# Optimization experiments

Hardware: AMD Instinct MI355X
Metric: run time of the kernel (lower is better)

Reference implementation:

```python
import jax, jax.numpy as jnp
import numpy as np

N = 50000          # nodes
M_UND = 500000     # undirected edges -> E = 2*M_UND directed messages
Q = 16             # num_groups
MAX_ITER = 10
BP_MAX_DIFF = 0.01


def setup_inputs() -> dict:
    key = jax.random.key(0)
    k1, k2, k3, k4 = jax.random.split(key, 4)
    u = jax.random.randint(k1, (M_UND,), 0, N)
    v = jax.random.randint(k2, (M_UND,), 0, N)
    # each undirected edge (u,v) yields directed messages u->v and v->u
    src = jnp.concatenate([u, v]).astype(jnp.int32)
    dst = jnp.concatenate([v, u]).astype(jnp.int32)
    rev = jnp.concatenate([jnp.arange(M_UND) + M_UND, jnp.arange(M_UND)]).astype(jnp.int32)
    psi0 = jax.random.uniform(k3, (N, Q), dtype=jnp.float32)
    psi0 = psi0 / psi0.sum(1, keepdims=True)
    msg0 = jax.random.uniform(k4, (2 * M_UND, Q), dtype=jnp.float32)
    msg0 = msg0 / msg0.sum(1, keepdims=True)
    c = 2.0 * M_UND / N  # mean degree
    beta = jnp.float32(np.log(Q / np.sqrt(c - 1.0) + 1.0))  # beta_ast init
    return dict(src=src, dst=dst, rev=rev, psi0=psi0, msg0=msg0, beta=beta, n_nodes=N)


def _bp_forward(src, dst, rev, psi0, msg0, beta, n_nodes):
    q = psi0.shape[1]
    n_edges = msg0.shape[0]
    mean_w = float(n_edges) / (float(n_nodes) * float(n_nodes))  # W.mean() for 0/1 weights
    expb_m1 = jnp.exp(beta) - 1.0
    h0 = (-beta * mean_w * psi0).sum(0)  # external field, shape [q]

    def step(carry, _):
        msg, psi, h, done = carry
        # S_e = 1 + psi_{src->dst} * (e^{beta*w} - 1), w == 1
        logS = jnp.log1p(msg * expb_m1)                                    # [E, q]
        node_log = jax.ops.segment_sum(logS, dst, num_segments=n_nodes)    # prod over incoming, log-domain
        # cavity update: message i->j uses all incoming to i except j->i (rev edge)
        new_msg = jax.nn.softmax(node_log[src] - logS[rev] + h, axis=-1)   # exp(h)*prod, normalized
        diff = jnp.max(jnp.abs(jax.lax.stop_gradient(new_msg) -
                               jax.lax.stop_gradient(msg)).sum(-1))
        logS2 = jnp.log1p(new_msg * expb_m1)
        node_log2 = jax.ops.segment_sum(logS2, dst, num_segments=n_nodes)
        new_psi = jax.nn.softmax(node_log2 + h, axis=-1)                    # marginals
        new_h = (-beta * mean_w * new_psi).sum(0)
        # freeze state once converged (mirrors early-return on max_diff < bp_max_diff)
        msg = jnp.where(done, msg, new_msg)
        psi = jnp.where(done, psi, new_psi)
        h = jnp.where(done, h, new_h)
        done = done | (diff < BP_MAX_DIFF)
        return (msg, psi, h, done), diff

    (msg, psi, h, done), _ = jax.lax.scan(
        step, (msg0, psi0, h0, jnp.array(False)), None, length=MAX_ITER)

    # soft modularity: (1/2m) sum_e psi_i . psi_j - sum_g (sum_i d_i psi_ig / 2m)^2
    m2 = float(n_edges)  # total directed edge weight (= 2m for unit weights)
    deg = jax.ops.segment_sum(jnp.ones((n_edges,), psi.dtype), dst, num_segments=n_nodes)
    edge_term = jnp.einsum('eq,eq->', psi[src], psi[dst]) / m2
    deg_term = jnp.sum((jnp.einsum('n,nq->q', deg, psi) / m2) ** 2)
    modularity = edge_term - deg_term
    # group-balance regularizer, scaled by sqrt(q) as in forward()
    reg = jnp.sum((psi.sum(0) / float(n_nodes) - 1.0 / q) ** 2) * np.sqrt(q)
    # mean per-node entropy of marginals, normalized by log(q)
    entropy_loss = jnp.mean(-jnp.sum(psi * jnp.log(psi + 1e-12), axis=-1)) / np.log(q)
    return psi, reg, entropy_loss, modularity


def reference(src, dst, rev, psi0, msg0, beta, n_nodes):
    return _bp_forward(src, dst, rev, psi0, msg0, beta, n_nodes)
```

## Files before the change

### kernel.cpp

```cpp
#include <hip/hip_runtime.h>

#define Q 16
#define SCAN_B 256

__device__ __forceinline__ float wsum(float v){
  #pragma unroll
  for(int o=32;o;o>>=1) v += __shfl_xor(v,o);
  return v;
}
__device__ __forceinline__ float wmaxr(float v){
  #pragma unroll
  for(int o=32;o;o>>=1) v = fmaxf(v,__shfl_xor(v,o));
  return v;
}

__global__ void __launch_bounds__(256, 4) k_edge(
    const int* __restrict__ src, const int* __restrict__ dst,
    const float* msg_in, float* msg_out,
    const float* __restrict__ nl, const float* __restrict__ hc,
    const float* __restrict__ betap,
    float* __restrict__ diffpart, const int* __restrict__ donep, int M)
{
  if (*donep) return;
  const float eb = __expf(*betap) - 1.0f;
  const int p = blockIdx.x*blockDim.x + threadIdx.x;
  float dloc = 0.0f;
  if (p < M) {
    const int u = src[p], v = dst[p];
    const float4* a  = (const float4*)(msg_in + (size_t)p*Q);
    const float4* b  = (const float4*)(msg_in + ((size_t)p + (size_t)M)*Q);
    const float4* h4 = (const float4*)hc;
    const float4* u4 = (const float4*)(nl + (size_t)u*Q);
    const float4* v4 = (const float4*)(nl + (size_t)v*Q);
    float4 a0=a[0], a1=a[1], a2=a[2], a3=a[3];
    float4 b0=b[0], b1=b[1], b2=b[2], b3=b[3];
    float4 h0=h4[0], h1=h4[1], h2=h4[2], h3=h4[3];
    float4 un0=u4[0], un1=u4[1], un2=u4[2], un3=u4[3];
    float4 vn0=v4[0], vn1=v4[1], vn2=v4[2], vn3=v4[3];
    float muv[Q], mvu[Q], hq[Q], nlu[Q], nlv[Q];
    #define UNP(arr,r0,r1,r2,r3) \
      arr[0]=r0.x;arr[1]=r0.y;arr[2]=r0.z;arr[3]=r0.w; \
      arr[4]=r1.x;arr[5]=r1.y;arr[6]=r1.z;arr[7]=r1.w; \
      arr[8]=r2.x;arr[9]=r2.y;arr[10]=r2.z;arr[11]=r2.w; \
      arr[12]=r3.x;arr[13]=r3.y;arr[14]=r3.z;arr[15]=r3.w;
    UNP(muv,a0,a1,a2,a3) UNP(mvu,b0,b1,b2,b3) UNP(hq,h0,h1,h2,h3)
    UNP(nlu,un0,un1,un2,un3) UNP(nlv,vn0,vn1,vn2,vn3)
    #undef UNP
    float tuv[Q], tvu[Q];
    #pragma unroll
    for (int q=0;q<Q;q++){
      float lsuv = __logf(fmaf(muv[q], eb, 1.0f));
      float lsvu = __logf(fmaf(mvu[q], eb, 1.0f));
      tuv[q] = nlu[q] - lsvu + hq[q];
      tvu[q] = nlv[q] - lsuv + hq[q];
    }
    float m1 = tuv[0], m2 = tvu[0];
    #pragma unroll
    for (int q=1;q<Q;q++){ m1=fmaxf(m1,tuv[q]); m2=fmaxf(m2,tvu[q]); }
    float s1=0.0f, s2=0.0f;
    #pragma unroll
    for (int q=0;q<Q;q++){
      tuv[q]=__expf(tuv[q]-m1); s1+=tuv[q];
      tvu[q]=__expf(tvu[q]-m2); s2+=tvu[q];
    }
    const float r1 = 1.0f/s1, r2 = 1.0f/s2;
    float d1=0.0f, d2=0.0f;
    #pragma unroll
    for (int q=0;q<Q;q++){
      float nuv = tuv[q]*r1, nvu = tvu[q]*r2;
      d1 += fabsf(nuv - muv[q]);
      d2 += fabsf(nvu - mvu[q]);
      muv[q]=nuv; mvu[q]=nvu;
    }
    dloc = fmaxf(d1,d2);
    float4* o1 = (float4*)(msg_out + (size_t)p*Q);
    float4* o2 = (float4*)(msg_out + ((size_t)p + (size_t)M)*Q);
    #pragma unroll
    for (int i=0;i<4;i++){
      o1[i] = make_float4(muv[4*i],muv[4*i+1],muv[4*i+2],muv[4*i+3]);
      o2[i] = make_float4(mvu[4*i],mvu[4*i+1],mvu[4*i+2],mvu[4*i+3]);
    }
  }
  __shared__ float smx[4];
  float wm = wmaxr(dloc);
  if ((threadIdx.x & 63) == 0) smx[threadIdx.x>>6] = wm;
  __syncthreads();
  if (threadIdx.x == 0)
    diffpart[blockIdx.x] = fmaxf(fmaxf(smx[0],smx[1]), fmaxf(smx[2],smx[3]));
}

__global__ void __launch_bounds__(256, 4) k_gather(
    const float* __restrict__ msg, const int* __restrict__ offs,
    const int* __restrict__ eid,
    float* __restrict__ nl, const float* __restrict__ hc,
    float* __restrict__ psi, const float* __restrict__ betap,
    const int* __restrict__ donep, float* __restrict__ hpart,
    int N, int mode)
{
  if (mode && *donep) return;
  const int wid = threadIdx.x >> 6;
  const int n = blockIdx.x*4 + wid;
  const float eb = __expf(*betap) - 1.0f;
  const int lane = threadIdx.x & 63;
  const int sub = lane >> 4, q = lane & 15;
  int start = 0, end = 0;
  if (n < N){ start = offs[n]; end = offs[n+1]; }
  float acc = 0.0f;
  int i = start + sub;
  for (; i + 4 < end; i += 8){
    const int e0 = eid[i], e1 = eid[i+4];
    const float x0 = msg[(size_t)e0*Q + q];
    const float x1 = msg[(size_t)e1*Q + q];
    acc += __logf(fmaf(x0, eb, 1.0f)) + __logf(fmaf(x1, eb, 1.0f));
  }
  if (i < end)
    acc += __logf(fmaf(msg[(size_t)eid[i]*Q + q], eb, 1.0f));
  acc += __shfl_xor(acc, 16);
  acc += __shfl_xor(acc, 32);
  if (n < N && sub == 0) nl[(size_t)n*Q + q] = acc;
  if (!mode) return;
  float t = acc + hc[q];
  float m = t;
  #pragma unroll
  for (int o=1;o<16;o<<=1) m = fmaxf(m, __shfl_xor(m,o));
  float ex = __expf(t-m);
  float s = ex;
  #pragma unroll
  for (int o=1;o<16;o<<=1) s += __shfl_xor(s,o);
  const float pq = ex/s;
  if (n < N && sub == 0) psi[(size_t)n*Q + q] = pq;
  __shared__ float smh[4][17];
  if (sub == 0) smh[wid][q] = (n < N) ? pq : 0.0f;
  __syncthreads();
  if (threadIdx.x < Q)
    hpart[(size_t)blockIdx.x*Q + threadIdx.x] =
      smh[0][threadIdx.x]+smh[1][threadIdx.x]+smh[2][threadIdx.x]+smh[3][threadIdx.x];
}

__global__ void __launch_bounds__(256) k_hred2(
    const float* __restrict__ hpart, int nrows,
    float* __restrict__ hpart2, int gH,
    const float* __restrict__ diffpart, int nbd,
    float* __restrict__ h, int* __restrict__ donep,
    int* __restrict__ cnt,
    const float* __restrict__ betap, float mean_w)
{
  if (*donep) return;
  const int t = threadIdx.x, g = t>>4, q = t&15;
  __shared__ float sm[16][17];
  {
    const int base = blockIdx.x*256;
    const int lim = min(base+256, nrows);
    float s = 0.0f;
    for (int r = base+g; r < lim; r += 16) s += hpart[(size_t)r*Q + q];
    sm[g][q] = s; __syncthreads();
    if (t < Q){
      float tot = 0.0f;
      #pragma unroll
      for (int i=0;i<16;i++) tot += sm[i][t];
      hpart2[(size_t)blockIdx.x*Q + t] = tot;
    }
  }
  __shared__ int amLast;
  __threadfence();
  if (t == 0) amLast = (atomicAdd(cnt, 1) == gH-1);
  __syncthreads();
  if (!amLast) return;
  {
    float s = 0.0f;
    for (int b = g; b < gH; b += 16) s += hpart2[(size_t)b*Q + q];
    __syncthreads();
    sm[g][q] = s; __syncthreads();
    if (t < Q){
      float tot = 0.0f;
      #pragma unroll
      for (int i=0;i<16;i++) tot += sm[i][t];
      h[t] = -(*betap) * mean_w * tot;
    }
  }
  float m = 0.0f;
  for (int i = t; i < nbd; i += 256) m = fmaxf(m, diffpart[i]);
  m = wmaxr(m);
  __shared__ float red[4];
  if ((t & 63) == 0) red[t>>6] = m;
  __syncthreads();
  if (t == 0 &&
      fmaxf(fmaxf(red[0],red[1]), fmaxf(red[2],red[3])) < 0.01f) *donep = 1;
}

__global__ void __launch_bounds__(256) k_h_part(
    const float* __restrict__ psi, float* __restrict__ hpart, int N)
{
  const int n = blockIdx.x*blockDim.x + threadIdx.x;
  float pv[Q];
  if (n < N) {
    const float4* a = (const float4*)(psi + (size_t)n*Q);
    #pragma unroll
    for (int i=0;i<4;i++){ float4 t=a[i]; pv[4*i]=t.x; pv[4*i+1]=t.y; pv[4*i+2]=t.z; pv[4*i+3]=t.w; }
  } else {
    #pragma unroll
    for (int q=0;q<Q;q++) pv[q]=0.0f;
  }
  __shared__ float sm[4][Q];
  const int wid = threadIdx.x>>6, lane = threadIdx.x&63;
  #pragma unroll
  for (int q=0;q<Q;q++){
    float s = wsum(pv[q]);
    if (lane == 0) sm[wid][q] = s;
  }
  __syncthreads();
  if (threadIdx.x < Q)
    hpart[(size_t)blockIdx.x*Q + threadIdx.x] =
      sm[0][threadIdx.x]+sm[1][threadIdx.x]+sm[2][threadIdx.x]+sm[3][threadIdx.x];
}

__global__ void __launch_bounds__(256) k_hfin(
    const float* __restrict__ hpart, float* __restrict__ h,
    const float* __restrict__ betap, int nb, float mean_w)
{
  const int t = threadIdx.x, g = t>>4, q = t&15;
  float s = 0.0f;
  for (int b = g; b < nb; b += 16) s += hpart[(size_t)b*Q + q];
  __shared__ float sm[16][17];
  sm[g][q] = s; __syncthreads();
  if (t < Q){
    float tot = 0.0f;
    #pragma unroll
    for (int i=0;i<16;i++) tot += sm[i][t];
    h[t] = -(*betap) * mean_w * tot;
  }
}

__global__ void __launch_bounds__(256) k_deg(
    const int* __restrict__ dst, int* __restrict__ deg, int E)
{
  const int e = blockIdx.x*blockDim.x + threadIdx.x;
  if (e < E) atomicAdd(&deg[dst[e]], 1);
}

__global__ void __launch_bounds__(SCAN_B) k_scan1(
    const int* __restrict__ deg, int* __restrict__ offs,
    int* __restrict__ bsum, int N)
{
  __shared__ int sm[SCAN_B];
  const int i = blockIdx.x*SCAN_B + threadIdx.x;
  const int v = (i<N) ? deg[i] : 0;
  sm[threadIdx.x] = v; __syncthreads();
  #pragma unroll
  for (int o=1;o<SCAN_B;o<<=1){
    int t = (threadIdx.x>=o) ? sm[threadIdx.x-o] : 0;
    __syncthreads();
    sm[threadIdx.x] += t;
    __syncthreads();
  }
  if (i<N) offs[i] = sm[threadIdx.x] - v;
  if (threadIdx.x==SCAN_B-1) bsum[blockIdx.x] = sm[threadIdx.x];
}

__global__ void __launch_bounds__(SCAN_B) k_scan2(int* __restrict__ bsum, int nb)
{
  __shared__ int sm[SCAN_B];
  const int v = (threadIdx.x<nb) ? bsum[threadIdx.x] : 0;
  sm[threadIdx.x] = v; __syncthreads();
  #pragma unroll
  for (int o=1;o<SCAN_B;o<<=1){
    int t = (threadIdx.x>=o) ? sm[threadIdx.x-o] : 0;
    __syncthreads();
    sm[threadIdx.x] += t;
    __syncthreads();
  }
  if (threadIdx.x<nb) bsum[threadIdx.x] = sm[threadIdx.x] - v;
}

__global__ void __launch_bounds__(SCAN_B) k_scan3(
    int* __restrict__ offs, int* __restrict__ cursor,
    const int* __restrict__ bsum, int N, int E)
{
  const int i = blockIdx.x*SCAN_B + threadIdx.x;
  if (i<N){
    const int o = offs[i] + bsum[blockIdx.x];
    offs[i] = o; cursor[i] = o;
  }
  if (i==0) offs[N] = E;
}

__global__ void __launch_bounds__(256) k_fill(
    const int* __restrict__ dst, int* __restrict__ cursor,
    int* __restrict__ eid, int E)
{
  const int e = blockIdx.x*blockDim.x + threadIdx.x;
  if (e < E){
    const int p = atomicAdd(&cursor[dst[e]], 1);
    eid[p] = e;
  }
}

__global__ void __launch_bounds__(256) k_edge_term(
    const int* __restrict__ src, const int* __restrict__ dst,
    const float* __restrict__ psi, float* __restrict__ edgepart, int M)
{
  const int p = blockIdx.x*blockDim.x + threadIdx.x;
  float d = 0.0f;
  if (p < M) {
    const int u = src[p], v = dst[p];
    const float4* a = (const float4*)(psi + (size_t)u*Q);
    const float4* b = (const float4*)(psi + (size_t)v*Q);
    #pragma unroll
    for (int i=0;i<4;i++){
      float4 x=a[i], y=b[i];
      d += x.x*y.x + x.y*y.y + x.z*y.z + x.w*y.w;
    }
    d *= 2.0f;
  }
  float s = wsum(d);
  __shared__ float sm[4];
  if ((threadIdx.x & 63) == 0) sm[threadIdx.x>>6] = s;
  __syncthreads();
  if (threadIdx.x == 0) edgepart[blockIdx.x] = sm[0]+sm[1]+sm[2]+sm[3];
}

__global__ void __launch_bounds__(256) k_node_stats(
    const float* __restrict__ psi, const int* __restrict__ deg,
    float* __restrict__ colpart, float* __restrict__ degpart,
    float* __restrict__ entpart, int N)
{
  const int n = blockIdx.x*blockDim.x + threadIdx.x;
  float pv[Q]; float dg = 0.0f; float ent = 0.0f;
  if (n < N) {
    const float4* a = (const float4*)(psi + (size_t)n*Q);
    #pragma unroll
    for (int i=0;i<4;i++){ float4 t=a[i]; pv[4*i]=t.x; pv[4*i+1]=t.y; pv[4*i+2]=t.z; pv[4*i+3]=t.w; }
    dg = (float)deg[n];
    #pragma unroll
    for (int q=0;q<Q;q++) ent -= pv[q]*__logf(pv[q]+1e-12f);
  } else {
    #pragma unroll
    for (int q=0;q<Q;q++) pv[q]=0.0f;
  }
  __shared__ float smc[4][Q], smd[4][Q], sme[4];
  const int wid = threadIdx.x>>6, lane = threadIdx.x&63;
  #pragma unroll
  for (int q=0;q<Q;q++){
    float s  = wsum(pv[q]);
    float s2 = wsum(pv[q]*dg);
    if (lane == 0){ smc[wid][q]=s; smd[wid][q]=s2; }
  }
  float se = wsum(ent);
  if (lane == 0) sme[wid] = se;
  __syncthreads();
  if (threadIdx.x < Q){
    colpart[(size_t)blockIdx.x*Q+threadIdx.x] =
      smc[0][threadIdx.x]+smc[1][threadIdx.x]+smc[2][threadIdx.x]+smc[3][threadIdx.x];
    degpart[(size_t)blockIdx.x*Q+threadIdx.x] =
      smd[0][threadIdx.x]+smd[1][threadIdx.x]+smd[2][threadIdx.x]+smd[3][threadIdx.x];
  }
  if (threadIdx.x == 0) entpart[blockIdx.x] = sme[0]+sme[1]+sme[2]+sme[3];
}

__global__ void __launch_bounds__(256) k_finalize(
    const float* __restrict__ edgepart, int ne,
    const float* __restrict__ colpart, const float* __restrict__ degpart,
    const float* __restrict__ entpart, int nbn,
    float* __restrict__ out, int N, float m2, int NQ)
{
  __shared__ float sm[16][Q];
  __shared__ float red[4];
  const int t = threadIdx.x, g = t>>4, q = t&15;
  float cs=0.0f, ds=0.0f;
  for (int b=g; b<nbn; b+=16){ cs += colpart[(size_t)b*Q+q]; ds += degpart[(size_t)b*Q+q]; }
  sm[g][q] = cs; __syncthreads();
  float colq = 0.0f;
  if (t < Q){ for (int i=0;i<16;i++) colq += sm[i][t]; }
  __syncthreads();
  sm[g][q] = ds; __syncthreads();
  float degq = 0.0f;
  if (t < Q){ for (int i=0;i<16;i++) degq += sm[i][t]; }
  __syncthreads();
  float es = 0.0f;
  for (int i=t; i<ne; i+=256) es += edgepart[i];
  es = wsum(es);
  if ((t&63)==0) red[t>>6] = es;
  __syncthreads();
  const float edge_total = red[0]+red[1]+red[2]+red[3];
  __syncthreads();
  float en = 0.0f;
  for (int i=t; i<nbn; i+=256) en += entpart[i];
  en = wsum(en);
  if ((t&63)==0) red[t>>6] = en;
  __syncthreads();
  const float ent_total = red[0]+red[1]+red[2]+red[3];
  __syncthreads();
  if (t < Q){ sm[0][t] = colq; sm[1][t] = degq; }
  __syncthreads();
  if (t == 0){
    float reg = 0.0f, dt = 0.0f;
    for (int i=0;i<Q;i++){
      float d = sm[0][i]/(float)N - 1.0f/(float)Q; reg += d*d;
      float s = sm[1][i]/m2; dt += s*s;
    }
    out[NQ+0] = reg * 4.0f;
    out[NQ+1] = ent_total/(float)N / 2.7725887222397811f;
    out[NQ+2] = edge_total/m2 - dt;
  }
}

extern "C" void kernel_launch(void* const* d_in, const int* in_sizes, int n_in,
                              void* d_out, int out_size, void* d_ws, size_t ws_size,
                              hipStream_t stream)
{
  const int*   src   = (const int*)  d_in[0];
  const int*   dst   = (const int*)  d_in[1];
  const float* psi0  = (const float*)d_in[3];
  const float* msg0  = (const float*)d_in[4];
  const float* betap = (const float*)d_in[5];

  const int E  = in_sizes[0];
  const int M  = E/2;
  const int NQ = in_sizes[3];
  const int N  = NQ/Q;
  const float mean_w = (float)((double)E/((double)N*(double)N));
  const float m2 = (float)E;

  const int B = 256;
  const int gE = (E+B-1)/B, gM = (M+B-1)/B, gN = (N+B-1)/B;
  const int nb = (N+SCAN_B-1)/SCAN_B;
  const int gW = (N+3)/4;
  const int gH = (gW+255)/256;

  char* w = (char*)d_ws;
  float* msgA    = (float*)w; w += (size_t)E*Q*sizeof(float);
  float* nl      = (float*)w; w += (size_t)NQ*sizeof(float);
  int*   eid     = (int*)  w; w += (size_t)E*sizeof(int);
  int*   offs    = (int*)  w; w += (size_t)(N+16)*sizeof(int);
  int*   cursor  = (int*)  w; w += (size_t)(N+16)*sizeof(int);
  int*   bsum    = (int*)  w; w += 256*sizeof(int);
  float* hpart   = (float*)w; w += (size_t)gW*Q*sizeof(float);
  float* hpart2  = (float*)w; w += (size_t)gH*Q*sizeof(float);
  float* diffpart= (float*)w; w += (size_t)gM*sizeof(float);
  float* edgepart= (float*)w; w += (size_t)gM*sizeof(float);
  float* colpart = (float*)w; w += (size_t)gN*Q*sizeof(float);
  float* degpart = (float*)w; w += (size_t)gN*Q*sizeof(float);
  float* entpart = (float*)w; w += (size_t)gN*sizeof(float);
  int*   deg     = (int*)  w; w += (size_t)(N+16)*sizeof(int);
  float* h       = (float*)w; w += 16*sizeof(float);
  int*   donep   = (int*)  w; w += 4*sizeof(int);
  int*   cnt     = (int*)  w; w += 16*sizeof(int);

  float* psi = (float*)d_out;

  const size_t small_bytes = (size_t)((char*)w - (char*)deg);
  hipMemsetAsync(deg, 0, small_bytes, stream);

  k_h_part<<<gN,B,0,stream>>>(psi0, hpart, N);
  k_hfin  <<<1, B,0,stream>>>(hpart, h, betap, gN, mean_w);
  k_deg   <<<gE,B,0,stream>>>(dst, deg, E);
  k_scan1 <<<nb,SCAN_B,0,stream>>>(deg, offs, bsum, N);
  k_scan2 <<<1, SCAN_B,0,stream>>>(bsum, nb);
  k_scan3 <<<nb,SCAN_B,0,stream>>>(offs, cursor, bsum, N, E);
  k_fill  <<<gE,B,0,stream>>>(dst, cursor, eid, E);
  k_gather<<<gW,B,0,stream>>>(msg0, offs, eid, nl, h, psi, betap, donep, hpart, N, 0);

  for (int k=0; k<10; ++k) {
    const float* mc = (k==0) ? msg0 : msgA;
    k_edge  <<<gM,B,0,stream>>>(src, dst, mc, msgA, nl, h, betap, diffpart, donep, M);
    k_gather<<<gW,B,0,stream>>>(msgA, offs, eid, nl, h, psi, betap, donep, hpart, N, 1);
    k_hred2 <<<gH,B,0,stream>>>(hpart, gW, hpart2, gH, diffpart, gM,
                                h, donep, &cnt[k], betap, mean_w);
  }

  k_edge_term <<<gM,B,0,stream>>>(src, dst, psi, edgepart, M);
  k_node_stats<<<gN,B,0,stream>>>(psi, deg, colpart, degpart, entpart, N);
  k_finalize  <<<1,B,0,stream>>>(edgepart, gM, colpart, degpart, entpart, gN,
                                 psi, N, m2, NQ);
}
```

Before: 1.153 ms.

## Store messages in destination-sorted CSR order and update edges with 16-lane groups

Messages now live in a buffer ordered by destination node. Each edge keeps its slot in that buffer, so the gather kernel reads messages contiguously with no eid indirection. The edge kernel now gives each undirected edge 16 lanes (one per group) in a grid-stride loop over a fixed grid. It does the softmax and diff with shuffles and writes both directions in place at their CSR slots. This removes the indirect, uncoalesced gather reads, but the edge kernel now does scattered 64-byte reads and writes through ipos, and there is a one-time scatter of msg0 into the new order.

```diff
diff --git a/kernel.cpp b/kernel.cpp
--- a/kernel.cpp
+++ b/kernel.cpp
@@ -14,72 +14,55 @@
   return v;
 }
 
-__global__ void __launch_bounds__(256, 4) k_edge(
+__global__ void __launch_bounds__(256, 4) k_edge16C(
     const int* __restrict__ src, const int* __restrict__ dst,
-    const float* msg_in, float* msg_out,
-    const float* __restrict__ nl, const float* __restrict__ hc,
+    const int* __restrict__ ipos,
+    float* msgC, const float* __restrict__ nl, const float* __restrict__ hc,
     const float* __restrict__ betap,
     float* __restrict__ diffpart, const int* __restrict__ donep, int M)
 {
   if (*donep) return;
   const float eb = __expf(*betap) - 1.0f;
-  const int p = blockIdx.x*blockDim.x + threadIdx.x;
+  const int q = threadIdx.x & 15;
+  const float hq = hc[q];
+  const int grp  = (blockIdx.x*blockDim.x + threadIdx.x) >> 4;
+  const int ngrp = (gridDim.x*blockDim.x) >> 4;
   float dloc = 0.0f;
-  if (p < M) {
+  for (int p = grp; p < M; p += ngrp){
     const int u = src[p], v = dst[p];
-    const float4* a  = (const float4*)(msg_in + (size_t)p*Q);
-    const float4* b  = (const float4*)(msg_in + ((size_t)p + (size_t)M)*Q);
-    const float4* h4 = (const float4*)hc;
-    const float4* u4 = (const float4*)(nl + (size_t)u*Q);
-    const float4* v4 = (const float4*)(nl + (size_t)v*Q);
-    float4 a0=a[0], a1=a[1], a2=a[2], a3=a[3];
-    float4 b0=b[0], b1=b[1], b2=b[2], b3=b[3];
-    float4 h0=h4[0], h1=h4[1], h2=h4[2], h3=h4[3];
-    float4 un0=u4[0], un1=u4[1], un2=u4[2], un3=u4[3];
-    float4 vn0=v4[0], vn1=v4[1], vn2=v4[2], vn3=v4[3];
-    float muv[Q], mvu[Q], hq[Q], nlu[Q], nlv[Q];
-    #define UNP(arr,r0,r1,r2,r3) \
-      arr[0]=r0.x;arr[1]=r0.y;arr[2]=r0.z;arr[3]=r0.w; \
-      arr[4]=r1.x;arr[5]=r1.y;arr[6]=r1.z;arr[7]=r1.w; \
-      arr[8]=r2.x;arr[9]=r2.y;arr[10]=r2.z;arr[11]=r2.w; \
-      arr[12]=r3.x;arr[13]=r3.y;arr[14]=r3.z;arr[15]=r3.w;
-    UNP(muv,a0,a1,a2,a3) UNP(mvu,b0,b1,b2,b3) UNP(hq,h0,h1,h2,h3)
-    UNP(nlu,un0,un1,un2,un3) UNP(nlv,vn0,vn1,vn2,vn3)
-    #undef UNP
-    float tuv[Q], tvu[Q];
-    #pragma unroll
-    for (int q=0;q<Q;q++){
-      float lsuv = __logf(fmaf(muv[q], eb, 1.0f));
-      float lsvu = __logf(fmaf(mvu[q], eb, 1.0f));
-      tuv[q] = nlu[q] - lsvu + hq[q];
-      tvu[q] = nlv[q] - lsuv + hq[q];
-    }
-    float m1 = tuv[0], m2 = tvu[0];
-    #pragma unroll
-    for (int q=1;q<Q;q++){ m1=fmaxf(m1,tuv[q]); m2=fmaxf(m2,tvu[q]); }
-    float s1=0.0f, s2=0.0f;
-    #pragma unroll
-    for (int q=0;q<Q;q++){
-      tuv[q]=__expf(tuv[q]-m1); s1+=tuv[q];
-      tvu[q]=__expf(tvu[q]-m2); s2+=tvu[q];
-    }
-    const float r1 = 1.0f/s1, r2 = 1.0f/s2;
-    float d1=0.0f, d2=0.0f;
-    #pragma unroll
-    for (int q=0;q<Q;q++){
-      float nuv = tuv[q]*r1, nvu = tvu[q]*r2;
-      d1 += fabsf(nuv - muv[q]);
-      d2 += fabsf(nvu - mvu[q]);
-      muv[q]=nuv; mvu[q]=nvu;
-    }
-    dloc = fmaxf(d1,d2);
-    float4* o1 = (float4*)(msg_out + (size_t)p*Q);
-    float4* o2 = (float4*)(msg_out + ((size_t)p + (size_t)M)*Q);
-    #pragma unroll
-    for (int i=0;i<4;i++){
-      o1[i] = make_float4(muv[4*i],muv[4*i+1],muv[4*i+2],muv[4*i+3]);
-      o2[i] = make_float4(mvu[4*i],mvu[4*i+1],mvu[4*i+2],mvu[4*i+3]);
-    }
+    const int ip0 = ipos[p];
+    const int ip1 = ipos[p + M];
+    const float muv = msgC[(size_t)ip0*Q + q];
+    const float mvu = msgC[(size_t)ip1*Q + q];
+    const float nlu = nl[(size_t)u*Q + q];
+    const float nlv = nl[(size_t)v*Q + q];
+    const float lsuv = __logf(fmaf(muv, eb, 1.0f));
+    const float lsvu = __logf(fmaf(mvu, eb, 1.0f));
+    float tuv = nlu - lsvu + hq;
+    float tvu = nlv - lsuv + hq;
+    float m1 = tuv, m2 = tvu;
+    #pragma unroll
+    for (int o=1;o<16;o<<=1){
+      m1 = fmaxf(m1, __shfl_xor(m1,o));
+      m2 = fmaxf(m2, __shfl_xor(m2,o));
+    }
+    const float e1 = __expf(tuv-m1), e2 = __expf(tvu-m2);
+    float s1 = e1, s2 = e2;
+    #pragma unroll
+    for (int o=1;o<16;o<<=1){
+      s1 += __shfl_xor(s1,o);
+      s2 += __shfl_xor(s2,o);
+    }
+    const float nuv = e1/s1, nvu = e2/s2;
+    float d1 = fabsf(nuv-muv), d2 = fabsf(nvu-mvu);
+    #pragma unroll
+    for (int o=1;o<16;o<<=1){
+      d1 += __shfl_xor(d1,o);
+      d2 += __shfl_xor(d2,o);
+    }
+    dloc = fmaxf(dloc, fmaxf(d1,d2));
+    msgC[(size_t)ip0*Q + q] = nuv;
+    msgC[(size_t)ip1*Q + q] = nvu;
   }
   __shared__ float smx[4];
   float wm = wmaxr(dloc);
@@ -89,9 +72,8 @@
     diffpart[blockIdx.x] = fmaxf(fmaxf(smx[0],smx[1]), fmaxf(smx[2],smx[3]));
 }
 
-__global__ void __launch_bounds__(256, 4) k_gather(
-    const float* __restrict__ msg, const int* __restrict__ offs,
-    const int* __restrict__ eid,
+__global__ void __launch_bounds__(256, 4) k_gatherC(
+    const float* __restrict__ msgC, const int* __restrict__ offs,
     float* __restrict__ nl, const float* __restrict__ hc,
     float* __restrict__ psi, const float* __restrict__ betap,
     const int* __restrict__ donep, float* __restrict__ hpart,
@@ -102,24 +84,22 @@
   const int n = blockIdx.x*4 + wid;
   const float eb = __expf(*betap) - 1.0f;
   const int lane = threadIdx.x & 63;
-  const int sub = lane >> 4, q = lane & 15;
+  const int sub = lane >> 4, q16 = lane & 15;
   int start = 0, end = 0;
   if (n < N){ start = offs[n]; end = offs[n+1]; }
   float acc = 0.0f;
   int i = start + sub;
   for (; i + 4 < end; i += 8){
-    const int e0 = eid[i], e1 = eid[i+4];
-    const float x0 = msg[(size_t)e0*Q + q];
-    const float x1 = msg[(size_t)e1*Q + q];
+    const float x0 = msgC[(size_t)i*Q + q16];
+    const float x1 = msgC[(size_t)(i+4)*Q + q16];
     acc += __logf(fmaf(x0, eb, 1.0f)) + __logf(fmaf(x1, eb, 1.0f));
   }
-  if (i < end)
-    acc += __logf(fmaf(msg[(size_t)eid[i]*Q + q], eb, 1.0f));
+  if (i < end) acc += __logf(fmaf(msgC[(size_t)i*Q + q16], eb, 1.0f));
   acc += __shfl_xor(acc, 16);
   acc += __shfl_xor(acc, 32);
-  if (n < N && sub == 0) nl[(size_t)n*Q + q] = acc;
+  if (n < N && sub == 0) nl[(size_t)n*Q + q16] = acc;
   if (!mode) return;
-  float t = acc + hc[q];
+  float t = acc + hc[q16];
   float m = t;
   #pragma unroll
   for (int o=1;o<16;o<<=1) m = fmaxf(m, __shfl_xor(m,o));
@@ -128,9 +108,9 @@
   #pragma unroll
   for (int o=1;o<16;o<<=1) s += __shfl_xor(s,o);
   const float pq = ex/s;
-  if (n < N && sub == 0) psi[(size_t)n*Q + q] = pq;
+  if (n < N && sub == 0) psi[(size_t)n*Q + q16] = pq;
   __shared__ float smh[4][17];
-  if (sub == 0) smh[wid][q] = (n < N) ? pq : 0.0f;
+  if (sub == 0) smh[wid][q16] = (n < N) ? pq : 0.0f;
   __syncthreads();
   if (threadIdx.x < Q)
     hpart[(size_t)blockIdx.x*Q + threadIdx.x] =
@@ -284,15 +264,25 @@
   if (i==0) offs[N] = E;
 }
 
-__global__ void __launch_bounds__(256) k_fill(
+__global__ void __launch_bounds__(256) k_fillC(
     const int* __restrict__ dst, int* __restrict__ cursor,
-    int* __restrict__ eid, int E)
+    int* __restrict__ ipos, int E)
 {
   const int e = blockIdx.x*blockDim.x + threadIdx.x;
-  if (e < E){
-    const int p = atomicAdd(&cursor[dst[e]], 1);
-    eid[p] = e;
-  }
+  if (e < E) ipos[e] = atomicAdd(&cursor[dst[e]], 1);
+}
+
+__global__ void __launch_bounds__(256) k_scatter0(
+    const float* __restrict__ msg0, const int* __restrict__ ipos,
+    float* __restrict__ msgC, int E)
+{
+  const int e = blockIdx.x*blockDim.x + threadIdx.x;
+  if (e >= E) return;
+  const int ip = ipos[e];
+  const float4* s = (const float4*)(msg0 + (size_t)e*Q);
+  float4* d = (float4*)(msgC + (size_t)ip*Q);
+  float4 x0=s[0], x1=s[1], x2=s[2], x3=s[3];
+  d[0]=x0; d[1]=x1; d[2]=x2; d[3]=x3;
 }
 
 __global__ void __launch_bounds__(256) k_edge_term(
@@ -424,19 +414,21 @@
   const int B = 256;
   const int gE = (E+B-1)/B, gM = (M+B-1)/B, gN = (N+B-1)/B;
   const int nb = (N+SCAN_B-1)/SCAN_B;
+  const int nbE = 2048;
   const int gW = (N+3)/4;
   const int gH = (gW+255)/256;
+  const int HPROWS = (gW > gN ? gW : gN);
 
   char* w = (char*)d_ws;
-  float* msgA    = (float*)w; w += (size_t)E*Q*sizeof(float);
+  float* msgC    = (float*)w; w += (size_t)E*Q*sizeof(float);
   float* nl      = (float*)w; w += (size_t)NQ*sizeof(float);
-  int*   eid     = (int*)  w; w += (size_t)E*sizeof(int);
+  int*   ipos    = (int*)  w; w += (size_t)E*sizeof(int);
   int*   offs    = (int*)  w; w += (size_t)(N+16)*sizeof(int);
   int*   cursor  = (int*)  w; w += (size_t)(N+16)*sizeof(int);
   int*   bsum    = (int*)  w; w += 256*sizeof(int);
-  float* hpart   = (float*)w; w += (size_t)gW*Q*sizeof(float);
+  float* hpart   = (float*)w; w += (size_t)HPROWS*Q*sizeof(float);
   float* hpart2  = (float*)w; w += (size_t)gH*Q*sizeof(float);
-  float* diffpart= (float*)w; w += (size_t)gM*sizeof(float);
+  float* diffpart= (float*)w; w += (size_t)nbE*sizeof(float);
   float* edgepart= (float*)w; w += (size_t)gM*sizeof(float);
   float* colpart = (float*)w; w += (size_t)gN*Q*sizeof(float);
   float* degpart = (float*)w; w += (size_t)gN*Q*sizeof(float);
@@ -451,21 +443,23 @@
   const size_t small_bytes = (size_t)((char*)w - (char*)deg);
   hipMemsetAsync(deg, 0, small_bytes, stream);
 
-  k_h_part<<<gN,B,0,stream>>>(psi0, hpart, N);
-  k_hfin  <<<1, B,0,stream>>>(hpart, h, betap, gN, mean_w);
-  k_deg   <<<gE,B,0,stream>>>(dst, deg, E);
-  k_scan1 <<<nb,SCAN_B,0,stream>>>(deg, offs, bsum, N);
-  k_scan2 <<<1, SCAN_B,0,stream>>>(bsum, nb);
-  k_scan3 <<<nb,SCAN_B,0,stream>>>(offs, cursor, bsum, N, E);
-  k_fill  <<<gE,B,0,stream>>>(dst, cursor, eid, E);
-  k_gather<<<gW,B,0,stream>>>(msg0, offs, eid, nl, h, psi, betap, donep, hpart, N, 0);
+  k_h_part  <<<gN,B,0,stream>>>(psi0, hpart, N);
+  k_hfin    <<<1, B,0,stream>>>(hpart, h, betap, gN, mean_w);
+  k_deg     <<<gE,B,0,stream>>>(dst, deg, E);
+  k_scan1   <<<nb,SCAN_B,0,stream>>>(deg, offs, bsum, N);
+  k_scan2   <<<1, SCAN_B,0,stream>>>(bsum, nb);
+  k_scan3   <<<nb,SCAN_B,0,stream>>>(offs, cursor, bsum, N, E);
+  k_fillC   <<<gE,B,0,stream>>>(dst, cursor, ipos, E);
+  k_scatter0<<<gE,B,0,stream>>>(msg0, ipos, msgC, E);
+  k_gatherC <<<gW,B,0,stream>>>(msgC, offs, nl, h, psi, betap, donep, hpart, N, 0);
 
   for (int k=0; k<10; ++k) {
-    const float* mc = (k==0) ? msg0 : msgA;
-    k_edge  <<<gM,B,0,stream>>>(src, dst, mc, msgA, nl, h, betap, diffpart, donep, M);
-    k_gather<<<gW,B,0,stream>>>(msgA, offs, eid, nl, h, psi, betap, donep, hpart, N, 1);
-    k_hred2 <<<gH,B,0,stream>>>(hpart, gW, hpart2, gH, diffpart, gM,
-                                h, donep, &cnt[k], betap, mean_w);
+    k_edge16C<<<nbE,B,0,stream>>>(src, dst, ipos, msgC, nl, h, betap,
+                                  diffpart, donep, M);
+    k_gatherC<<<gW,B,0,stream>>>(msgC, offs, nl, h, psi, betap, donep,
+                                 hpart, N, 1);
+    k_hred2  <<<gH,B,0,stream>>>(hpart, gW, hpart2, gH, diffpart, nbE,
+                                 h, donep, &cnt[k], betap, mean_w);
   }
 
   k_edge_term <<<gM,B,0,stream>>>(src, dst, psi, edgepart, M);
```

New measurement: 1.023 ms. -11.3%, faster.
